# Optimization experiments

Measured on AMD Instinct MI355X. Metric: run time of the kernel, lower is better.

The kernel has to match this reference:

```python
import jax, jax.numpy as jnp
import numpy as np

FEATS = 768
HEAD = 12
HD = FEATS // HEAD


def setup_inputs() -> dict:
    key = jax.random.key(0)
    ks = jax.random.split(key, 10)
    b, n, f = 8, 1024, FEATS
    s = 1.0 / np.sqrt(f)
    return {
        "x": jax.random.normal(ks[0], (b, n, f), dtype=jnp.float32),
        "bias": jnp.zeros((), dtype=jnp.float32),
        "Wq": jax.random.normal(ks[1], (f, f), dtype=jnp.float32) * s,
        "bq": jnp.zeros((f,), dtype=jnp.float32),
        "Wk": jax.random.normal(ks[2], (f, f), dtype=jnp.float32) * s,
        "bk": jnp.zeros((f,), dtype=jnp.float32),
        "Wv": jax.random.normal(ks[3], (f, f), dtype=jnp.float32) * s,
        "bv": jnp.zeros((f,), dtype=jnp.float32),
        "Wo": jax.random.normal(ks[4], (f, f), dtype=jnp.float32) * s,
        "bo": jnp.zeros((f,), dtype=jnp.float32),
    }


def reference(x, bias, Wq, bq, Wk, bk, Wv, bv, Wo, bo):
    b, n, f = x.shape
    sqrt_d = jnp.sqrt(jnp.asarray(f, dtype=x.dtype))  # scale uses full feats, per source

    def split_heads(t):  # (b,n,f) -> (b,h,n,hd)
        return t.reshape(b, n, HEAD, HD).transpose(0, 2, 1, 3)

    q = split_heads(x @ Wq.T + bq)
    k = split_heads(x @ Wk.T + bk)
    v = split_heads(x @ Wv.T + bv)

    # sigmoid attention: no row-wise normalization
    score = jax.nn.sigmoid(jnp.einsum('bhif,bhjf->bhij', q, k) / sqrt_d + bias)
    attn = jnp.einsum('bhij,bhjf->bihf', score, v)  # (b,n,h,hd)
    o = attn.reshape(b, n, f) @ Wo.T + bo  # dropout p=0.0 -> identity
    return o
```

## Files before the change

kernel.cpp:

```cpp
#include <hip/hip_runtime.h>

#define FEATS 768
#define NHEAD 12
#define HD    64
#define SEQ   1024
#define NB    8
#define MROWS (NB*SEQ)
#define NQK   (2*FEATS)
#define QKVN  (3*FEATS)
#define QSC   0.0520616136f

typedef __attribute__((ext_vector_type(8))) __bf16          bf16x8;
typedef __attribute__((ext_vector_type(4))) __bf16          bf16x4;
typedef __attribute__((ext_vector_type(4))) unsigned short  us4;
typedef __attribute__((ext_vector_type(4))) float           f32x4;

__device__ __forceinline__ unsigned short f2bf(float f) {
  union { float f; unsigned u; } v; v.f = f;
  return (unsigned short)((v.u + 0x7fffu + ((v.u >> 16) & 1u)) >> 16);
}

__device__ __forceinline__ void gload_lds16(const void* g, void* l) {
  __builtin_amdgcn_global_load_lds(
      (const __attribute__((address_space(1))) void*)g,
      (__attribute__((address_space(3))) void*)l, 16, 0, 0);
}

__global__ void cast_all(const float* __restrict__ Wq, const float* __restrict__ Wk,
                         const float* __restrict__ Wv, const float* __restrict__ Wo,
                         const float* __restrict__ bq, const float* __restrict__ bk,
                         const float* __restrict__ bv,
                         unsigned short* __restrict__ Wcat,
                         unsigned short* __restrict__ Wobf,
                         float* __restrict__ bcat) {
  int blk = blockIdx.x;
  if (blk < 2304) {
    int mtx = blk / 576;
    int i = (blk % 576) * 256 + threadIdx.x;
    const float* src = (mtx == 0) ? Wq : (mtx == 1) ? Wk : (mtx == 2) ? Wv : Wo;
    f32x4 v = ((const f32x4*)src)[i];
    us4 o;
    o[0] = f2bf(v[0]); o[1] = f2bf(v[1]); o[2] = f2bf(v[2]); o[3] = f2bf(v[3]);
    if (mtx < 3) ((us4*)Wcat)[mtx * 147456 + i] = o;
    else         ((us4*)Wobf)[i] = o;
  } else {
    int i = (blk - 2304) * 256 + threadIdx.x;
    if (i < QKVN)
      bcat[i] = (i < FEATS) ? bq[i] : (i < 2*FEATS ? bk[i-FEATS] : bv[i-2*FEATS]);
  }
}

#define FOFF(row) ((row)*64 + (((g) ^ (((row) >> 1) & 3)) << 4))

__global__ __launch_bounds__(256, 3) void gemm1_bt(
    const float* __restrict__ X,
    const unsigned short* __restrict__ B,
    const float* __restrict__ bias,
    unsigned short* __restrict__ QKo,
    unsigned short* __restrict__ VTo)
{
  __shared__ __align__(16) char Al[2 * 8192];
  __shared__ __align__(16) char Bl[3 * 12288];

  const int tid  = threadIdx.x;
  const int lane = tid & 63;
  const int w    = tid >> 6;
  const int l15  = lane & 15;
  const int g    = lane >> 4;
  const int wm   = (w >> 1) * 64;
  const int wn   = (w & 1) * 96;

  const int id  = blockIdx.x;
  const int xcd = id & 7;
  const int j   = id >> 3;
  const int mi  = xcd * 8 + (j & 7);
  const int ni  = j >> 3;
  const int mbase = mi * 128;
  const int nbase = ni * 192;

  const int trow  = tid >> 2;
  const int sslot = ((tid & 3) ^ ((tid >> 3) & 3)) * 8;
  const float*          Ag = X + (size_t)(mbase + trow) * 768 + sslot;
  const unsigned short* Bg = B + (size_t)(nbase + trow) * 768 + sslot;

  f32x4 ar[4];

  auto LOAD_A = [&](int t) {
    const float* sa = Ag + t * 32;
    ar[0] = *(const f32x4*)(sa);
    ar[1] = *(const f32x4*)(sa + 4);
    ar[2] = *(const f32x4*)(sa + 64*768);
    ar[3] = *(const f32x4*)(sa + 64*768 + 4);
  };
  auto WRITE_A = [&](int buf) {
    char* da = Al + buf * 8192 + tid * 16;
    us4 o0, o1;
#pragma unroll
    for (int k = 0; k < 4; k++) { o0[k] = f2bf(ar[0][k]); }
#pragma unroll
    for (int k = 0; k < 4; k++) { o1[k] = f2bf(ar[1][k]); }
    *(us4*)(da)     = o0;
    *(us4*)(da + 8) = o1;
#pragma unroll
    for (int k = 0; k < 4; k++) { o0[k] = f2bf(ar[2][k]); }
#pragma unroll
    for (int k = 0; k < 4; k++) { o1[k] = f2bf(ar[3][k]); }
    *(us4*)(da + 4096)     = o0;
    *(us4*)(da + 4096 + 8) = o1;
  };
  auto STAGE_B = [&](int buf, int t) {
    const unsigned short* sb = Bg + t * 32;
    char* db = Bl + buf * 12288 + tid * 16;
    gload_lds16(sb,            db);
    gload_lds16(sb + 64*768,   db + 4096);
    gload_lds16(sb + 128*768,  db + 8192);
  };

  f32x4 acc[4][6] = {};

  LOAD_A(0);
  STAGE_B(0, 0);
  STAGE_B(1, 1);
  WRITE_A(0);
  asm volatile("s_waitcnt vmcnt(3)" ::: "memory");
  asm volatile("s_waitcnt lgkmcnt(0)" ::: "memory");
  __builtin_amdgcn_s_barrier();

  for (int t = 0; t < 24; t++) {
    if (t < 23) LOAD_A(t + 1);
    if (t < 22) STAGE_B((t + 2) % 3, t + 2);

    const char* Ab = Al + (t & 1) * 8192;
    const char* Bb = Bl + (t % 3) * 12288;
    bf16x8 af[4];
#pragma unroll
    for (int mf = 0; mf < 4; mf++) {
      const int row = wm + mf*16 + l15;
      af[mf] = *(const bf16x8*)(Ab + FOFF(row));
    }
    __builtin_amdgcn_s_setprio(1);
#pragma unroll
    for (int nf = 0; nf < 6; nf++) {
      const int row = wn + nf*16 + l15;
      bf16x8 bfv = *(const bf16x8*)(Bb + FOFF(row));
#pragma unroll
      for (int mf = 0; mf < 4; mf++)
        acc[mf][nf] = __builtin_amdgcn_mfma_f32_16x16x32_bf16(af[mf], bfv, acc[mf][nf], 0, 0, 0);
    }
    __builtin_amdgcn_s_setprio(0);

    if (t < 23) {
      WRITE_A((t + 1) & 1);
      asm volatile("s_waitcnt vmcnt(3)" ::: "memory");
      asm volatile("s_waitcnt lgkmcnt(0)" ::: "memory");
      __builtin_amdgcn_s_barrier();
    }
  }

  const bool isQK = (ni < 8);
  const float osc = (ni < 4) ? QSC : 1.0f;
#pragma unroll
  for (int mf = 0; mf < 4; mf++)
#pragma unroll
    for (int nf = 0; nf < 6; nf++) {
      const int col  = nbase + wn + nf*16 + l15;
      const float bb = bias[col];
      const int row0 = mbase + wm + mf*16 + g*4;
      if (isQK) {
#pragma unroll
        for (int r = 0; r < 4; r++)
          QKo[(size_t)(row0 + r)*NQK + col] = f2bf((acc[mf][nf][r] + bb) * osc);
      } else {
        const int c  = col - NQK;
        const int hh = c >> 6, dd = c & 63;
        const int bI = row0 >> 10, n0 = row0 & 1023;
        const int rl  = n0 & 63;
        const int cp  = ((rl >> 5) << 5) | (((rl >> 2) & 3) << 3) | (((rl >> 4) & 1) << 2);
        const int n0p = (n0 & ~63) | cp;
        us4 o;
#pragma unroll
        for (int r = 0; r < 4; r++) o[r] = f2bf(acc[mf][nf][r] + bb);
        *(us4*)(VTo + ((size_t)((bI*NHEAD + hh)*HD + dd))*SEQ + n0p) = o;
      }
    }
}

__global__ __launch_bounds__(256, 4) void gemm2_bt(
    const unsigned short* __restrict__ A,
    const unsigned short* __restrict__ B,
    const float* __restrict__ bias,
    float* __restrict__ C)
{
  __shared__ __align__(16) char Al[2 * 4096];
  __shared__ __align__(16) char Bl[3 * 8192];

  const int tid  = threadIdx.x;
  const int lane = tid & 63;
  const int w    = tid >> 6;
  const int l15  = lane & 15;
  const int g    = lane >> 4;
  const int wm   = (w >> 1) * 32;
  const int wn   = (w & 1) * 64;

  const int id  = blockIdx.x;
  const int xcd = id & 7;
  const int j   = id >> 3;
  const int mi  = xcd * 16 + (j & 15);
  const int ni  = j >> 4;
  const int mbase = mi * 64;
  const int nbase = ni * 128;

  const int trow  = tid >> 2;
  const int sslot = ((tid & 3) ^ ((tid >> 3) & 3)) * 8;
  const unsigned short* Ag = A + (size_t)(mbase + trow) * 768 + sslot;
  const unsigned short* Bg = B + (size_t)(nbase + trow) * 768 + sslot;

  auto STAGE_A = [&](int buf, int t) {
    char* da = Al + buf * 4096 + tid * 16;
    gload_lds16(Ag + t * 32, da);
  };
  auto STAGE_B = [&](int buf, int t) {
    const unsigned short* sb = Bg + t * 32;
    char* db = Bl + buf * 8192 + tid * 16;
    gload_lds16(sb,           db);
    gload_lds16(sb + 64*768,  db + 4096);
  };

  f32x4 acc[2][4] = {};

  STAGE_A(0, 0);
  STAGE_B(0, 0);
  STAGE_B(1, 1);
  asm volatile("s_waitcnt vmcnt(2)" ::: "memory");
  __builtin_amdgcn_s_barrier();

  for (int t = 0; t < 24; t++) {
    if (t < 23) STAGE_A((t + 1) & 1, t + 1);
    if (t < 22) STAGE_B((t + 2) % 3, t + 2);

    const char* Ab = Al + (t & 1) * 4096;
    const char* Bb = Bl + (t % 3) * 8192;
    bf16x8 af[2], bfv[4];
#pragma unroll
    for (int mf = 0; mf < 2; mf++) {
      const int row = wm + mf*16 + l15;
      af[mf] = *(const bf16x8*)(Ab + FOFF(row));
    }
#pragma unroll
    for (int nf = 0; nf < 4; nf++) {
      const int row = wn + nf*16 + l15;
      bfv[nf] = *(const bf16x8*)(Bb + FOFF(row));
    }
    __builtin_amdgcn_s_setprio(1);
#pragma unroll
    for (int mf = 0; mf < 2; mf++)
#pragma unroll
      for (int nf = 0; nf < 4; nf++)
        acc[mf][nf] = __builtin_amdgcn_mfma_f32_16x16x32_bf16(af[mf], bfv[nf], acc[mf][nf], 0, 0, 0);
    __builtin_amdgcn_s_setprio(0);

    if (t < 23) {
      if (t < 22) asm volatile("s_waitcnt vmcnt(2)" ::: "memory");
      else        asm volatile("s_waitcnt vmcnt(0)" ::: "memory");
      __builtin_amdgcn_s_barrier();
    }
  }

#pragma unroll
  for (int mf = 0; mf < 2; mf++)
#pragma unroll
    for (int nf = 0; nf < 4; nf++) {
      const int col  = nbase + wn + nf*16 + l15;
      const float bb = bias[col];
      const int row0 = mbase + wm + mf*16 + g*4;
#pragma unroll
      for (int r = 0; r < 4; r++)
        C[(size_t)(row0 + r)*FEATS + col] = acc[mf][nf][r] + bb;
    }
}
#undef FOFF

__global__ __launch_bounds__(256, 3) void attn_kernel(
    const unsigned short* __restrict__ QK,
    const unsigned short* __restrict__ VT,
    const float* __restrict__ biasp,
    unsigned short* __restrict__ AO)
{
  __shared__ __align__(16) char Kl[2][8192];
  __shared__ __align__(16) char Vl[2][8192];

  const int tid  = threadIdx.x;
  const int lane = tid & 63;
  const int w    = tid >> 6;
  const int l15  = lane & 15;
  const int g    = lane >> 4;

  const int id  = blockIdx.x;
  const int r8  = id & 7;
  const int m   = id >> 3;
  const int bh  = r8 * 12 + (m >> 3);
  const int qx  = m & 7;
  const int b   = bh / NHEAD;
  const int h   = bh % NHEAD;
  const int rowB  = b * SEQ;
  const int qbase = rowB + qx * 128;

  const float Kb = __builtin_amdgcn_exp2f(-biasp[0] * 1.4426950408889634f);

  bf16x8 qf[2][2];
  {
    const unsigned short* qp = QK + (size_t)(qbase + w*32 + l15) * NQK + h*HD + g*8;
    qf[0][0] = *(const bf16x8*)(qp);
    qf[0][1] = *(const bf16x8*)(qp + 32);
    qf[1][0] = *(const bf16x8*)(qp + 16*NQK);
    qf[1][1] = *(const bf16x8*)(qp + 16*NQK + 32);
  }

  const int trow = tid >> 3;
  const int colb = ((tid & 7) * 16) ^ ((trow & 7) << 4);
  const char* Ksrc = (const char*)QK +
      ((size_t)(rowB + trow) * NQK + FEATS + h*HD) * 2 + colb;
  const char* Vsrc = (const char*)VT +
      ((size_t)(bh*HD + trow)) * (SEQ*2) + colb;

  auto STAGE_K = [&](int p, int t) {
    char* kw = Kl[p] + tid*16;
    gload_lds16(Ksrc + (size_t)t * 64 * (NQK*2),              kw);
    gload_lds16(Ksrc + (size_t)t * 64 * (NQK*2) + 32*(NQK*2), kw + 4096);
  };
  auto STAGE_V = [&](int p, int t) {
    char* vw = Vl[p] + tid*16;
    gload_lds16(Vsrc + t * 128,              vw);
    gload_lds16(Vsrc + t * 128 + 32*(SEQ*2), vw + 4096);
  };

  f32x4 o_acc[4][2] = {};
  f32x4 sE[2][4], sO[2][4];

  auto SIGPV = [&](f32x4 (&sP)[2][4], const char* Vp) {
    bf16x8 paq[2][2];
#pragma unroll
    for (int qm = 0; qm < 2; qm++) {
      float sg[4][4];
#pragma unroll
      for (int nf = 0; nf < 4; nf++)
#pragma unroll
        for (int rr = 0; rr < 4; rr++) {
          const float e = __builtin_amdgcn_exp2f(-sP[qm][nf][rr]);
          sg[nf][rr] = __builtin_amdgcn_rcpf(__builtin_fmaf(Kb, e, 1.0f));
        }
#pragma unroll
      for (int js = 0; js < 2; js++) {
        bf16x8 pa;
#pragma unroll
        for (int jj = 0; jj < 4; jj++) {
          pa[jj]     = (__bf16)sg[2*js][jj];
          pa[jj + 4] = (__bf16)sg[2*js + 1][jj];
        }
        paq[qm][js] = pa;
      }
    }
#pragma unroll
    for (int js = 0; js < 2; js++) {
      bf16x8 vf[4];
#pragma unroll
      for (int df = 0; df < 4; df++) {
        const int row = df*16 + l15;
        const int by  = (row*128 + js*64 + g*16) ^ ((row & 7) << 4);
        vf[df] = *(const bf16x8*)(Vp + by);
      }
      __builtin_amdgcn_s_setprio(1);
#pragma unroll
      for (int df = 0; df < 4; df++)
#pragma unroll
        for (int qm = 0; qm < 2; qm++)
          o_acc[df][qm] = __builtin_amdgcn_mfma_f32_16x16x32_bf16(vf[df], paq[qm][js], o_acc[df][qm], 0, 0, 0);
      __builtin_amdgcn_s_setprio(0);
    }
  };

  auto BODY = [&](int t, f32x4 (&sC)[2][4], f32x4 (&sP)[2][4], bool stK, bool doPrev) {
    if (stK) STAGE_K((t + 1) & 1, t + 1);
    STAGE_V(t & 1, t);

    const char* Kp = Kl[t & 1];
#pragma unroll
    for (int qm = 0; qm < 2; qm++)
#pragma unroll
      for (int nf = 0; nf < 4; nf++)
        sC[qm][nf] = (f32x4){0.f, 0.f, 0.f, 0.f};
    __builtin_amdgcn_s_setprio(1);
#pragma unroll
    for (int nf = 0; nf < 4; nf++)
#pragma unroll
      for (int ks = 0; ks < 2; ks++) {
        const int row = nf*16 + l15;
        const int by  = (row*128 + ks*64 + g*16) ^ ((row & 7) << 4);
        bf16x8 kf = *(const bf16x8*)(Kp + by);
        sC[0][nf] = __builtin_amdgcn_mfma_f32_16x16x32_bf16(kf, qf[0][ks], sC[0][nf], 0, 0, 0);
        sC[1][nf] = __builtin_amdgcn_mfma_f32_16x16x32_bf16(kf, qf[1][ks], sC[1][nf], 0, 0, 0);
      }
    __builtin_amdgcn_s_setprio(0);

    if (doPrev) SIGPV(sP, Vl[(t - 1) & 1]);

    __syncthreads();
  };

  STAGE_K(0, 0);
  __syncthreads();

  BODY(0, sE, sO, true, false);
#pragma unroll 1
  for (int t = 1; t < 15; t += 2) {
    BODY(t,     sO, sE, true, true);
    BODY(t + 1, sE, sO, true, true);
  }
  BODY(15, sO, sE, false, true);
  SIGPV(sO, Vl[1]);

  unsigned short* aop = AO + (size_t)(qbase + w*32) * FEATS + h*HD;
#pragma unroll
  for (int df = 0; df < 4; df++)
#pragma unroll
    for (int qm = 0; qm < 2; qm++) {
      const int q  = qm*16 + l15;
      const int d0 = df*16 + g*4;
      bf16x4 o;
#pragma unroll
      for (int rr = 0; rr < 4; rr++) o[rr] = (__bf16)o_acc[df][qm][rr];
      *(bf16x4*)(aop + (size_t)q * FEATS + d0) = o;
    }
}

extern "C" void kernel_launch(void* const* d_in, const int* in_sizes, int n_in,
                              void* d_out, int out_size, void* d_ws, size_t ws_size,
                              hipStream_t stream) {
  const float* x    = (const float*)d_in[0];
  const float* bias = (const float*)d_in[1];
  const float* Wq   = (const float*)d_in[2];
  const float* bq   = (const float*)d_in[3];
  const float* Wk   = (const float*)d_in[4];
  const float* bk   = (const float*)d_in[5];
  const float* Wv   = (const float*)d_in[6];
  const float* bv   = (const float*)d_in[7];
  const float* Wo   = (const float*)d_in[8];
  const float* bo   = (const float*)d_in[9];
  float* out = (float*)d_out;

  char* ws = (char*)d_ws;
  unsigned short* Xbf  = (unsigned short*)(ws + 0);
  unsigned short* Wcat = (unsigned short*)(ws + 12582912);
  unsigned short* Wobf = (unsigned short*)(ws + 16121856);
  float*          bcat = (float*)        (ws + 17301504);
  unsigned short* QKb  = (unsigned short*)(ws + 17310720);
  unsigned short* VTb  = (unsigned short*)(ws + 42476544);
  unsigned short* AO   = Xbf;

  cast_all<<<2313, 256, 0, stream>>>(Wq, Wk, Wv, Wo, bq, bk, bv,
                                     Wcat, Wobf, bcat);

  gemm1_bt<<<768, 256, 0, stream>>>(x, Wcat, bcat, QKb, VTb);

  attn_kernel<<<768, 256, 0, stream>>>(QKb, VTb, bias, AO);

  gemm2_bt<<<768, 256, 0, stream>>>(AO, Wobf, bo, out);
}
```

Before: 105.0 us.

## Double-buffer A prefetch registers and unroll GEMM main loop by two

In the projection GEMM, A tiles are now held in two register sets (even and odd) so global loads run two k-steps ahead. Each tile is converted and written to LDS at the start of the step that needs it, not after the compute. The main loop is unrolled by two with explicit vmcnt waits adjusted for the extra in-flight loads. This aims to hide global-load latency of the fp32 A tile behind MFMA work, at the cost of about 32 more VGPRs, which may lower occupancy.

Result: no change. 106.8 us (+1.7%).

```diff
diff --git a/kernel.cpp b/kernel.cpp
--- a/kernel.cpp
+++ b/kernel.cpp
@@ -83,16 +83,16 @@
   const float*          Ag = X + (size_t)(mbase + trow) * 768 + sslot;
   const unsigned short* Bg = B + (size_t)(nbase + trow) * 768 + sslot;
 
-  f32x4 ar[4];
-
-  auto LOAD_A = [&](int t) {
+  f32x4 arE[4], arO[4];
+
+  auto LOAD_A = [&](f32x4 (&ar)[4], int t) {
     const float* sa = Ag + t * 32;
     ar[0] = *(const f32x4*)(sa);
     ar[1] = *(const f32x4*)(sa + 4);
     ar[2] = *(const f32x4*)(sa + 64*768);
     ar[3] = *(const f32x4*)(sa + 64*768 + 4);
   };
-  auto WRITE_A = [&](int buf) {
+  auto WRITE_A = [&](f32x4 (&ar)[4], int buf) {
     char* da = Al + buf * 8192 + tid * 16;
     us4 o0, o1;
 #pragma unroll
@@ -118,40 +118,52 @@
 
   f32x4 acc[4][6] = {};
 
-  LOAD_A(0);
+  auto COMPUTE = [&](int t) {
+    const char* Ab = Al + (t & 1) * 8192;
+    const char* Bb = Bl + (t % 3) * 12288;
+    bf16x8 af[4];
+#pragma unroll
+    for (int mf = 0; mf < 4; mf++) {
+      const int row = wm + mf*16 + l15;
+      af[mf] = *(const bf16x8*)(Ab + FOFF(row));
+    }
+    __builtin_amdgcn_s_setprio(1);
+#pragma unroll
+    for (int nf = 0; nf < 6; nf++) {
+      const int row = wn + nf*16 + l15;
+      bf16x8 bfv = *(const bf16x8*)(Bb + FOFF(row));
+#pragma unroll
+      for (int mf = 0; mf < 4; mf++)
+        acc[mf][nf] = __builtin_amdgcn_mfma_f32_16x16x32_bf16(af[mf], bfv, acc[mf][nf], 0, 0, 0);
+    }
+    __builtin_amdgcn_s_setprio(0);
+  };
+
+  LOAD_A(arE, 0);
+  LOAD_A(arO, 1);
   STAGE_B(0, 0);
   STAGE_B(1, 1);
-  WRITE_A(0);
+  WRITE_A(arE, 0);
   asm volatile("s_waitcnt vmcnt(3)" ::: "memory");
   asm volatile("s_waitcnt lgkmcnt(0)" ::: "memory");
   __builtin_amdgcn_s_barrier();
 
-  for (int t = 0; t < 24; t++) {
-    if (t < 23) LOAD_A(t + 1);
-    if (t < 22) STAGE_B((t + 2) % 3, t + 2);
-
-    const char* Ab = Al + (t & 1) * 8192;
-    const char* Bb = Bl + (t % 3) * 12288;
-    bf16x8 af[4];
-#pragma unroll
-    for (int mf = 0; mf < 4; mf++) {
-      const int row = wm + mf*16 + l15;
-      af[mf] = *(const bf16x8*)(Ab + FOFF(row));
-    }
-    __builtin_amdgcn_s_setprio(1);
-#pragma unroll
-    for (int nf = 0; nf < 6; nf++) {
-      const int row = wn + nf*16 + l15;
-      bf16x8 bfv = *(const bf16x8*)(Bb + FOFF(row));
-#pragma unroll
-      for (int mf = 0; mf < 4; mf++)
-        acc[mf][nf] = __builtin_amdgcn_mfma_f32_16x16x32_bf16(af[mf], bfv, acc[mf][nf], 0, 0, 0);
-    }
-    __builtin_amdgcn_s_setprio(0);
-
-    if (t < 23) {
-      WRITE_A((t + 1) & 1);
-      asm volatile("s_waitcnt vmcnt(3)" ::: "memory");
+#pragma unroll 1
+  for (int t = 0; t < 24; t += 2) {
+    WRITE_A(arO, 1);
+    if (t < 22) { LOAD_A(arE, t + 2); STAGE_B((t + 2) % 3, t + 2); }
+    COMPUTE(t);
+    if (t < 22) asm volatile("s_waitcnt vmcnt(7)" ::: "memory");
+    else        asm volatile("s_waitcnt vmcnt(0)" ::: "memory");
+    asm volatile("s_waitcnt lgkmcnt(0)" ::: "memory");
+    __builtin_amdgcn_s_barrier();
+
+    const int u = t + 1;
+    if (u < 23) WRITE_A(arE, 0);
+    if (u < 22) { LOAD_A(arO, u + 2); STAGE_B((u + 2) % 3, u + 2); }
+    COMPUTE(u);
+    if (u < 22) asm volatile("s_waitcnt vmcnt(7)" ::: "memory");
+    if (u < 23) {
       asm volatile("s_waitcnt lgkmcnt(0)" ::: "memory");
       __builtin_amdgcn_s_barrier();
     }
```
